# Optimization experiments

Measured on AMD Instinct MI355X. Metric: run time of the kernel, lower is better.

Reference implementation:

```python
import jax, jax.numpy as jnp
import numpy as np

N_NODES = 100000
N_EDGES = 1600000
D = 64


def setup_inputs() -> dict:
    key = jax.random.key(0)
    k0, k1, k2, k3 = jax.random.split(key, 4)
    x = jax.random.normal(k0, (N_NODES, D), dtype=jnp.float32)
    edge_index = jax.random.randint(k1, (2, N_EDGES), 0, N_NODES, dtype=jnp.int64)
    W1 = jax.random.normal(k2, (D, D), dtype=jnp.float32) * 0.1
    b1 = jnp.zeros((D,), dtype=jnp.float32)
    W2 = jax.random.normal(k3, (D, D), dtype=jnp.float32) * 0.1
    b2 = jnp.zeros((D,), dtype=jnp.float32)
    return {"x": x, "edge_index": edge_index, "W1": W1, "b1": b1, "W2": W2, "b2": b2}


def _gcn_layer(x, edge_index, W, b):
    n = x.shape[0]
    h = x @ W  # [N, Dout] -- transform before aggregation (small GEMM)
    loop = jnp.arange(n, dtype=edge_index.dtype)
    src = jnp.concatenate([edge_index[0], loop])
    dst = jnp.concatenate([edge_index[1], loop])
    deg = jax.ops.segment_sum(jnp.ones_like(dst, dtype=h.dtype), dst, num_segments=n)
    dinv = jax.lax.rsqrt(deg)  # deg >= 1 thanks to self loops
    norm = dinv[src] * dinv[dst]  # [E+N]
    msg = h[src] * norm[:, None]  # gather: [E+N, Dout]
    agg = jax.ops.segment_sum(msg, dst, num_segments=n)  # scatter-add
    return agg + b


def reference(x, edge_index, W1, b1, W2, b2):
    # dropout p = 0.0 -> identity
    h = jax.nn.relu(_gcn_layer(x, edge_index, W1, b1))
    h = jax.nn.relu(_gcn_layer(h, edge_index, W2, b2))
    return h
```

## Files before the change

### kernel.cpp

```cpp
#include <hip/hip_runtime.h>
#include <hip/hip_bf16.h>

#define D 64
#define NB_HIST 256
#define MAXBK 512

typedef float vfloat4 __attribute__((ext_vector_type(4)));

__device__ __forceinline__ unsigned short f2bf(float f) {
    union { float f; unsigned u; } v; v.f = f;
    unsigned r = (v.u + 0x7FFF + ((v.u >> 16) & 1)) >> 16;
    return (unsigned short)r;
}
__device__ __forceinline__ float bflo(unsigned u) {
    union { unsigned u; float f; } v; v.u = u << 16; return v.f;
}
__device__ __forceinline__ float bfhi(unsigned u) {
    union { unsigned u; float f; } v; v.u = u & 0xFFFF0000u; return v.f;
}

__global__ __launch_bounds__(256) void passA_gemm(
    const int* __restrict__ dst, int* __restrict__ blockCounts, int E, int per, int NBK,
    const float* __restrict__ X, const float* __restrict__ W,
    unsigned short* __restrict__ hn, int N)
{
    int tid = threadIdx.x;

    if ((int)blockIdx.x < NB_HIST) {
        __shared__ int hist[MAXBK];
        for (int i = tid; i < NBK; i += 256) hist[i] = 0;
        __syncthreads();
        int lo = blockIdx.x * per, hi = min(E, lo + per);
        for (int i = lo + tid * 4; i < hi; i += 1024) {
            if (i + 3 < hi) {
                int4 d4 = *(const int4*)(dst + i);
                atomicAdd(&hist[d4.x >> 8], 1);
                atomicAdd(&hist[d4.y >> 8], 1);
                atomicAdd(&hist[d4.z >> 8], 1);
                atomicAdd(&hist[d4.w >> 8], 1);
            } else {
                for (int k = i; k < hi; ++k) atomicAdd(&hist[dst[k] >> 8], 1);
            }
        }
        __syncthreads();
        for (int i = tid; i < NBK; i += 256)
            blockCounts[(size_t)blockIdx.x * NBK + i] = hist[i];
        return;
    }

    __shared__ float sW[D * D];
    __shared__ float sX[32 * D];
    int rowBase = ((int)blockIdx.x - NB_HIST) * 32;

    for (int i = tid; i < 1024; i += 256)
        ((vfloat4*)sW)[i] = ((const vfloat4*)W)[i];
    for (int i = tid; i < 512; i += 256) {
        int r = rowBase + (i >> 4);
        vfloat4 v = (vfloat4)0.0f;
        if (r < N) v = __builtin_nontemporal_load(((const vfloat4*)X) + rowBase * 16 + i);
        ((vfloat4*)sX)[i] = v;
    }
    __syncthreads();

    int wave = tid >> 6, lane = tid & 63;
    float accv[8];
#pragma unroll
    for (int r = 0; r < 8; ++r) accv[r] = 0.0f;
    int xoff = (wave * 8) * D;
#pragma unroll 8
    for (int k = 0; k < D; ++k) {
        float wv = sW[k * D + lane];
#pragma unroll
        for (int r = 0; r < 8; ++r)
            accv[r] += sX[xoff + r * D + k] * wv;
    }
#pragma unroll
    for (int r = 0; r < 8; ++r) {
        int row = rowBase + wave * 8 + r;
        if (row < N) hn[(size_t)row * D + lane] = f2bf(accv[r]);
    }
}

__global__ __launch_bounds__(256) void scan_cols(
    const int* __restrict__ blockCounts, int* __restrict__ partial,
    int* __restrict__ totals, int NBK)
{
    int wave = threadIdx.x >> 6, lane = threadIdx.x & 63;
    int k = blockIdx.x * 4 + wave;
    if (k >= NBK) return;
    int carry = 0;
    for (int base = 0; base < NB_HIST; base += 64) {
        int b = base + lane;
        int v = blockCounts[(size_t)b * NBK + k];
        int inc = v;
        for (int d = 1; d < 64; d <<= 1) {
            int t = __shfl_up(inc, d, 64);
            if (lane >= d) inc += t;
        }
        partial[(size_t)k * NB_HIST + b] = inc - v + carry;
        carry += __shfl(inc, 63, 64);
    }
    if (lane == 0) totals[k] = carry;
}

__global__ void scan_buckets(const int* __restrict__ totals, int* __restrict__ bofs, int NBK) {
    int lane = threadIdx.x;
    int carry = 0;
    for (int base = 0; base < NBK; base += 64) {
        int i = base + lane;
        int v = (i < NBK) ? totals[i] : 0;
        int inc = v;
        for (int d = 1; d < 64; d <<= 1) {
            int t = __shfl_up(inc, d, 64);
            if (lane >= d) inc += t;
        }
        if (i < NBK) bofs[i] = inc - v + carry;
        carry += __shfl(inc, 63, 64);
    }
}

__global__ __launch_bounds__(256) void passB(
    const int* __restrict__ src, const int* __restrict__ dst,
    const int* __restrict__ bofs, const int* __restrict__ partial,
    int* __restrict__ bucketed, int E, int per, int NBK)
{
    __shared__ int cur[MAXBK];
    int tid = threadIdx.x, b = blockIdx.x;
    for (int i = tid; i < NBK; i += 256)
        cur[i] = bofs[i] + partial[(size_t)i * NB_HIST + b];
    __syncthreads();
    int lo = b * per, hi = min(E, lo + per);
    for (int i = lo + tid * 4; i < hi; i += 1024) {
        if (i + 3 < hi) {
            int4 d4 = *(const int4*)(dst + i);
            int4 s4 = *(const int4*)(src + i);
            int p0 = atomicAdd(&cur[d4.x >> 8], 1);
            int p1 = atomicAdd(&cur[d4.y >> 8], 1);
            int p2 = atomicAdd(&cur[d4.z >> 8], 1);
            int p3 = atomicAdd(&cur[d4.w >> 8], 1);
            bucketed[p0] = (s4.x << 8) | (d4.x & 255);
            bucketed[p1] = (s4.y << 8) | (d4.y & 255);
            bucketed[p2] = (s4.z << 8) | (d4.z & 255);
            bucketed[p3] = (s4.w << 8) | (d4.w & 255);
        } else {
            for (int k = i; k < hi; ++k) {
                int d = dst[k], s = src[k];
                int pos = atomicAdd(&cur[d >> 8], 1);
                bucketed[pos] = (s << 8) | (d & 255);
            }
        }
    }
}

__global__ __launch_bounds__(256) void build_csr_scale(
    const int* __restrict__ bucketed, const int* __restrict__ bofs,
    const int* __restrict__ totals, int* __restrict__ deg, float* __restrict__ dinv,
    int* __restrict__ ofs, int* __restrict__ csr,
    unsigned short* __restrict__ hn, int N)
{
    __shared__ int h[256];
    __shared__ int scn[256];
    __shared__ float sdv[256];
    int tid = threadIdx.x, k = blockIdx.x;
    int e0 = bofs[k], e1 = e0 + totals[k];
    int node = k * 256 + tid;

    h[tid] = 0;
    __syncthreads();
    for (int i = e0 + tid; i < e1; i += 256)
        atomicAdd(&h[bucketed[i] & 255], 1);
    __syncthreads();

    int mydeg = h[tid];
    scn[tid] = mydeg;
    __syncthreads();
    for (int d2 = 1; d2 < 256; d2 <<= 1) {
        int t = (tid >= d2) ? scn[tid - d2] : 0;
        __syncthreads();
        scn[tid] += t;
        __syncthreads();
    }
    int myofs = scn[tid] - mydeg;

    float dv = rsqrtf((float)(mydeg + 1));
    sdv[tid] = dv;
    if (node < N) {
        deg[node]  = mydeg;
        dinv[node] = dv;
        ofs[node]  = e0 + myofs;
    }

    h[tid] = myofs;
    __syncthreads();
    for (int i = e0 + tid; i < e1; i += 256) {
        int v = bucketed[i];
        int pos = atomicAdd(&h[v & 255], 1);
        csr[e0 + pos] = v >> 8;
    }

    __syncthreads();
    int4* hp = (int4*)hn;
    for (int c = tid; c < 2048; c += 256) {
        int r = c >> 3;
        int n2 = k * 256 + r;
        if (n2 < N) {
            float f = sdv[r];
            size_t idx = (size_t)n2 * 8 + (c & 7);
            int4 hv = hp[idx];
            unsigned r0 = (unsigned)f2bf(bflo(hv.x) * f) | ((unsigned)f2bf(bfhi(hv.x) * f) << 16);
            unsigned r1 = (unsigned)f2bf(bflo(hv.y) * f) | ((unsigned)f2bf(bfhi(hv.y) * f) << 16);
            unsigned r2 = (unsigned)f2bf(bflo(hv.z) * f) | ((unsigned)f2bf(bfhi(hv.z) * f) << 16);
            unsigned r3 = (unsigned)f2bf(bflo(hv.w) * f) | ((unsigned)f2bf(bfhi(hv.w) * f) << 16);
            hp[idx] = make_int4((int)r0, (int)r1, (int)r2, (int)r3);
        }
    }
}

__global__ __launch_bounds__(256) void gemm2(
    const unsigned short* __restrict__ h1b, const float* __restrict__ W,
    const float* __restrict__ dinv, unsigned short* __restrict__ hn, int N)
{
    __shared__ float sW[D * D];
    __shared__ float sX[32 * D];
    int tid = threadIdx.x;
    int rowBase = blockIdx.x * 32;

    for (int i = tid; i < 1024; i += 256)
        ((vfloat4*)sW)[i] = ((const vfloat4*)W)[i];
    {
        int r = tid >> 3, c8 = tid & 7;
        int row = rowBase + r;
        int4 hv = make_int4(0, 0, 0, 0);
        if (row < N) hv = ((const int4*)h1b)[(size_t)row * 8 + c8];
        float* dst8 = &sX[r * D + c8 * 8];
        dst8[0] = bflo(hv.x); dst8[1] = bfhi(hv.x);
        dst8[2] = bflo(hv.y); dst8[3] = bfhi(hv.y);
        dst8[4] = bflo(hv.z); dst8[5] = bfhi(hv.z);
        dst8[6] = bflo(hv.w); dst8[7] = bfhi(hv.w);
    }
    __syncthreads();

    int wave = tid >> 6, lane = tid & 63;
    float accv[8];
#pragma unroll
    for (int r = 0; r < 8; ++r) accv[r] = 0.0f;
    int xoff = (wave * 8) * D;
#pragma unroll 8
    for (int k = 0; k < D; ++k) {
        float wv = sW[k * D + lane];
#pragma unroll
        for (int r = 0; r < 8; ++r)
            accv[r] += sX[xoff + r * D + k] * wv;
    }
#pragma unroll
    for (int r = 0; r < 8; ++r) {
        int row = rowBase + wave * 8 + r;
        if (row < N) hn[(size_t)row * D + lane] = f2bf(accv[r] * dinv[row]);
    }
}

template <bool BF16OUT>
__global__ __launch_bounds__(256) void aggregate_relu(
    const int* __restrict__ ofs, const int* __restrict__ deg,
    const int* __restrict__ csr, const unsigned short* __restrict__ hn,
    const float* __restrict__ dinv, const float* __restrict__ bias,
    void* __restrict__ outv, int N)
{
    int t    = blockIdx.x * 256 + threadIdx.x;
    int lane = threadIdx.x & 63;
    int grp  = lane >> 3, sub = lane & 7;
    int node = (t >> 6) * 8 + grp;
    bool live = (node < N);

    const int4* hrow = (const int4*)hn;
    float2 a0 = {0.f, 0.f}, a1 = {0.f, 0.f}, a2 = {0.f, 0.f}, a3 = {0.f, 0.f};

    int s0 = 0, cnt = 0;
    if (live) {
        s0  = ofs[node];
        cnt = deg[node];
        int4 h = hrow[(size_t)node * 8 + sub];
        a0.x += bflo(h.x); a0.y += bfhi(h.x);
        a1.x += bflo(h.y); a1.y += bfhi(h.y);
        a2.x += bflo(h.z); a2.y += bfhi(h.z);
        a3.x += bflo(h.w); a3.y += bfhi(h.w);
    }

    const int* cp = csr + s0;
    int j = 0;
    for (; j + 3 < cnt; j += 4) {
        int sA = cp[j], sB = cp[j + 1], sC = cp[j + 2], sD = cp[j + 3];
        int4 hA = hrow[(size_t)sA * 8 + sub];
        int4 hB = hrow[(size_t)sB * 8 + sub];
        int4 hC = hrow[(size_t)sC * 8 + sub];
        int4 hD = hrow[(size_t)sD * 8 + sub];
        a0.x += bflo(hA.x); a0.y += bfhi(hA.x);
        a1.x += bflo(hA.y); a1.y += bfhi(hA.y);
        a2.x += bflo(hA.z); a2.y += bfhi(hA.z);
        a3.x += bflo(hA.w); a3.y += bfhi(hA.w);
        a0.x += bflo(hB.x); a0.y += bfhi(hB.x);
        a1.x += bflo(hB.y); a1.y += bfhi(hB.y);
        a2.x += bflo(hB.z); a2.y += bfhi(hB.z);
        a3.x += bflo(hB.w); a3.y += bfhi(hB.w);
        a0.x += bflo(hC.x); a0.y += bfhi(hC.x);
        a1.x += bflo(hC.y); a1.y += bfhi(hC.y);
        a2.x += bflo(hC.z); a2.y += bfhi(hC.z);
        a3.x += bflo(hC.w); a3.y += bfhi(hC.w);
        a0.x += bflo(hD.x); a0.y += bfhi(hD.x);
        a1.x += bflo(hD.y); a1.y += bfhi(hD.y);
        a2.x += bflo(hD.z); a2.y += bfhi(hD.z);
        a3.x += bflo(hD.w); a3.y += bfhi(hD.w);
    }
    for (; j < cnt; ++j) {
        int sA = cp[j];
        int4 hA = hrow[(size_t)sA * 8 + sub];
        a0.x += bflo(hA.x); a0.y += bfhi(hA.x);
        a1.x += bflo(hA.y); a1.y += bfhi(hA.y);
        a2.x += bflo(hA.z); a2.y += bfhi(hA.z);
        a3.x += bflo(hA.w); a3.y += bfhi(hA.w);
    }

    if (live) {
        float dw = dinv[node];
        float4 b0 = ((const float4*)bias)[sub * 2];
        float4 b1 = ((const float4*)bias)[sub * 2 + 1];
        float o0 = fmaxf(a0.x * dw + b0.x, 0.f);
        float o1 = fmaxf(a0.y * dw + b0.y, 0.f);
        float o2 = fmaxf(a1.x * dw + b0.z, 0.f);
        float o3 = fmaxf(a1.y * dw + b0.w, 0.f);
        float o4 = fmaxf(a2.x * dw + b1.x, 0.f);
        float o5 = fmaxf(a2.y * dw + b1.y, 0.f);
        float o6 = fmaxf(a3.x * dw + b1.z, 0.f);
        float o7 = fmaxf(a3.y * dw + b1.w, 0.f);
        if (BF16OUT) {
            unsigned r0 = (unsigned)f2bf(o0) | ((unsigned)f2bf(o1) << 16);
            unsigned r1 = (unsigned)f2bf(o2) | ((unsigned)f2bf(o3) << 16);
            unsigned r2 = (unsigned)f2bf(o4) | ((unsigned)f2bf(o5) << 16);
            unsigned r3 = (unsigned)f2bf(o6) | ((unsigned)f2bf(o7) << 16);
            ((int4*)outv)[(size_t)node * 8 + sub] =
                make_int4((int)r0, (int)r1, (int)r2, (int)r3);
        } else {
            float4 v0 = make_float4(o0, o1, o2, o3);
            float4 v1 = make_float4(o4, o5, o6, o7);
            ((float4*)outv)[(size_t)node * 16 + sub * 2]     = v0;
            ((float4*)outv)[(size_t)node * 16 + sub * 2 + 1] = v1;
        }
    }
}


extern "C" void kernel_launch(void* const* d_in, const int* in_sizes, int n_in,
                              void* d_out, int out_size, void* d_ws, size_t ws_size,
                              hipStream_t stream) {
    const float* x   = (const float*)d_in[0];
    const int*   ei  = (const int*)d_in[1];
    const float* W1  = (const float*)d_in[2];
    const float* b1  = (const float*)d_in[3];
    const float* W2  = (const float*)d_in[4];
    const float* b2  = (const float*)d_in[5];

    int N = in_sizes[0] / D;
    int E = in_sizes[1] / 2;
    const int* src = ei;
    const int* dst = ei + E;
    int NBK = (N + 255) >> 8;
    int per = (((E + NB_HIST - 1) / NB_HIST) + 3) & ~3;

    char* ws = (char*)d_ws;
    int*            blockCounts = (int*)(ws + 0x00000000);
    int*            partial     = (int*)(ws + 0x00080000);
    int*            totals      = (int*)(ws + 0x00100000);
    int*            bofs        = (int*)(ws + 0x00110000);
    int*            deg         = (int*)(ws + 0x00120000);
    float*          dinv        = (float*)(ws + 0x00190000);
    int*            ofs         = (int*)(ws + 0x00200000);
    int*            bucketed    = (int*)(ws + 0x00280000);
    int*            csr         = (int*)(ws + 0x00A00000);
    unsigned short* hn          = (unsigned short*)(ws + 0x01100000);
    unsigned short* h1b         = (unsigned short*)(ws + 0x01D80000);
    float*          outF        = (float*)d_out;

    int nb_G = (N + 31) / 32;
    int nb_A = (N + 31) / 32;

    passA_gemm<<<NB_HIST + nb_G, 256, 0, stream>>>(dst, blockCounts, E, per, NBK, x, W1, hn, N);
    scan_cols<<<(NBK + 3) / 4, 256, 0, stream>>>(blockCounts, partial, totals, NBK);
    scan_buckets<<<1, 64, 0, stream>>>(totals, bofs, NBK);
    passB<<<NB_HIST, 256, 0, stream>>>(src, dst, bofs, partial, bucketed, E, per, NBK);
    build_csr_scale<<<NBK, 256, 0, stream>>>(bucketed, bofs, totals, deg, dinv, ofs, csr, hn, N);

    aggregate_relu<true><<<nb_A, 256, 0, stream>>>(ofs, deg, csr, hn, dinv, b1, (void*)h1b, N);
    gemm2<<<nb_G, 256, 0, stream>>>(h1b, W2, dinv, hn, N);
    aggregate_relu<false><<<nb_A, 256, 0, stream>>>(ofs, deg, csr, hn, dinv, b2, (void*)outF, N);
}
```

Measured before the change: 240.1 us.

## Fuse scans via last-block counter, split CSR histogram by src tile, vectorize GEMM

```diff
diff --git a/kernel.cpp b/kernel.cpp
--- a/kernel.cpp
+++ b/kernel.cpp
@@ -4,6 +4,7 @@
 #define D 64
 #define NB_HIST 256
 #define MAXBK 512
+#define NT 16
 
 typedef float vfloat4 __attribute__((ext_vector_type(4)));
 
@@ -20,13 +21,15 @@
 }
 
 __global__ __launch_bounds__(256) void passA_gemm(
-    const int* __restrict__ dst, int* __restrict__ blockCounts, int E, int per, int NBK,
+    const int* __restrict__ dst, int* __restrict__ blockCounts, int* __restrict__ ctr,
+    int E, int per, int NBK,
     const float* __restrict__ X, const float* __restrict__ W,
     unsigned short* __restrict__ hn, int N)
 {
     int tid = threadIdx.x;
 
     if ((int)blockIdx.x < NB_HIST) {
+        if (blockIdx.x == 0 && tid == 0) *ctr = 0;
         __shared__ int hist[MAXBK];
         for (int i = tid; i < NBK; i += 256) hist[i] = 0;
         __syncthreads();
@@ -67,12 +70,17 @@
 #pragma unroll
     for (int r = 0; r < 8; ++r) accv[r] = 0.0f;
     int xoff = (wave * 8) * D;
-#pragma unroll 8
-    for (int k = 0; k < D; ++k) {
-        float wv = sW[k * D + lane];
-#pragma unroll
-        for (int r = 0; r < 8; ++r)
-            accv[r] += sX[xoff + r * D + k] * wv;
+#pragma unroll 4
+    for (int k = 0; k < D; k += 4) {
+        float w0 = sW[k * D + lane];
+        float w1 = sW[(k + 1) * D + lane];
+        float w2 = sW[(k + 2) * D + lane];
+        float w3 = sW[(k + 3) * D + lane];
+#pragma unroll
+        for (int r = 0; r < 8; ++r) {
+            vfloat4 xv = *(const vfloat4*)&sX[xoff + r * D + k];
+            accv[r] += xv.x * w0 + xv.y * w1 + xv.z * w2 + xv.w * w3;
+        }
     }
 #pragma unroll
     for (int r = 0; r < 8; ++r) {
@@ -81,41 +89,47 @@
     }
 }
 
-__global__ __launch_bounds__(256) void scan_cols(
+__global__ __launch_bounds__(256) void scan_all(
     const int* __restrict__ blockCounts, int* __restrict__ partial,
-    int* __restrict__ totals, int NBK)
-{
+    int* __restrict__ totals, int* __restrict__ bofs, int* __restrict__ ctr, int NBK)
+{
+    __shared__ int slast;
     int wave = threadIdx.x >> 6, lane = threadIdx.x & 63;
     int k = blockIdx.x * 4 + wave;
-    if (k >= NBK) return;
-    int carry = 0;
-    for (int base = 0; base < NB_HIST; base += 64) {
-        int b = base + lane;
-        int v = blockCounts[(size_t)b * NBK + k];
-        int inc = v;
-        for (int d = 1; d < 64; d <<= 1) {
-            int t = __shfl_up(inc, d, 64);
-            if (lane >= d) inc += t;
-        }
-        partial[(size_t)k * NB_HIST + b] = inc - v + carry;
-        carry += __shfl(inc, 63, 64);
-    }
-    if (lane == 0) totals[k] = carry;
-}
-
-__global__ void scan_buckets(const int* __restrict__ totals, int* __restrict__ bofs, int NBK) {
-    int lane = threadIdx.x;
-    int carry = 0;
-    for (int base = 0; base < NBK; base += 64) {
-        int i = base + lane;
-        int v = (i < NBK) ? totals[i] : 0;
-        int inc = v;
-        for (int d = 1; d < 64; d <<= 1) {
-            int t = __shfl_up(inc, d, 64);
-            if (lane >= d) inc += t;
-        }
-        if (i < NBK) bofs[i] = inc - v + carry;
-        carry += __shfl(inc, 63, 64);
+    if (k < NBK) {
+        int carry = 0;
+        for (int base = 0; base < NB_HIST; base += 64) {
+            int b = base + lane;
+            int v = blockCounts[(size_t)b * NBK + k];
+            int inc = v;
+            for (int d = 1; d < 64; d <<= 1) {
+                int t = __shfl_up(inc, d, 64);
+                if (lane >= d) inc += t;
+            }
+            partial[(size_t)k * NB_HIST + b] = inc - v + carry;
+            carry += __shfl(inc, 63, 64);
+        }
+        if (lane == 0) totals[k] = carry;
+    }
+    __syncthreads();
+    __threadfence();
+    if (threadIdx.x == 0)
+        slast = (atomicAdd(ctr, 1) == (int)gridDim.x - 1) ? 1 : 0;
+    __syncthreads();
+    if (slast && wave == 0) {
+        __threadfence();
+        int carry = 0;
+        for (int base = 0; base < NBK; base += 64) {
+            int i = base + lane;
+            int v = (i < NBK) ? totals[i] : 0;
+            int inc = v;
+            for (int d = 1; d < 64; d <<= 1) {
+                int t = __shfl_up(inc, d, 64);
+                if (lane >= d) inc += t;
+            }
+            if (i < NBK) bofs[i] = inc - v + carry;
+            carry += __shfl(inc, 63, 64);
+        }
     }
 }
 
@@ -158,20 +172,28 @@
     int* __restrict__ ofs, int* __restrict__ csr,
     unsigned short* __restrict__ hn, int N)
 {
-    __shared__ int h[256];
+    __shared__ int h2[NT * 256];
     __shared__ int scn[256];
     __shared__ float sdv[256];
     int tid = threadIdx.x, k = blockIdx.x;
     int e0 = bofs[k], e1 = e0 + totals[k];
     int node = k * 256 + tid;
 
-    h[tid] = 0;
-    __syncthreads();
-    for (int i = e0 + tid; i < e1; i += 256)
-        atomicAdd(&h[bucketed[i] & 255], 1);
-    __syncthreads();
-
-    int mydeg = h[tid];
+    for (int i = tid; i < NT * 256; i += 256) h2[i] = 0;
+    __syncthreads();
+    for (int i = e0 + tid; i < e1; i += 256) {
+        int v = bucketed[i];
+        atomicAdd(&h2[((v >> 21) << 8) | (v & 255)], 1);
+    }
+    __syncthreads();
+
+    int pre[NT];
+    int mydeg = 0;
+#pragma unroll
+    for (int t2 = 0; t2 < NT; ++t2) {
+        pre[t2] = mydeg;
+        mydeg += h2[(t2 << 8) | tid];
+    }
     scn[tid] = mydeg;
     __syncthreads();
     for (int d2 = 1; d2 < 256; d2 <<= 1) {
@@ -190,11 +212,13 @@
         ofs[node]  = e0 + myofs;
     }
 
-    h[tid] = myofs;
+#pragma unroll
+    for (int t2 = 0; t2 < NT; ++t2)
+        h2[(t2 << 8) | tid] = myofs + pre[t2];
     __syncthreads();
     for (int i = e0 + tid; i < e1; i += 256) {
         int v = bucketed[i];
-        int pos = atomicAdd(&h[v & 255], 1);
+        int pos = atomicAdd(&h2[((v >> 21) << 8) | (v & 255)], 1);
         csr[e0 + pos] = v >> 8;
     }
 
@@ -245,12 +269,17 @@
 #pragma unroll
     for (int r = 0; r < 8; ++r) accv[r] = 0.0f;
     int xoff = (wave * 8) * D;
-#pragma unroll 8
-    for (int k = 0; k < D; ++k) {
-        float wv = sW[k * D + lane];
-#pragma unroll
-        for (int r = 0; r < 8; ++r)
-            accv[r] += sX[xoff + r * D + k] * wv;
+#pragma unroll 4
+    for (int k = 0; k < D; k += 4) {
+        float w0 = sW[k * D + lane];
+        float w1 = sW[(k + 1) * D + lane];
+        float w2 = sW[(k + 2) * D + lane];
+        float w3 = sW[(k + 3) * D + lane];
+#pragma unroll
+        for (int r = 0; r < 8; ++r) {
+            vfloat4 xv = *(const vfloat4*)&sX[xoff + r * D + k];
+            accv[r] += xv.x * w0 + xv.y * w1 + xv.z * w2 + xv.w * w3;
+        }
     }
 #pragma unroll
     for (int r = 0; r < 8; ++r) {
@@ -371,6 +400,7 @@
     int*            partial     = (int*)(ws + 0x00080000);
     int*            totals      = (int*)(ws + 0x00100000);
     int*            bofs        = (int*)(ws + 0x00110000);
+    int*            ctr         = (int*)(ws + 0x00118000);
     int*            deg         = (int*)(ws + 0x00120000);
     float*          dinv        = (float*)(ws + 0x00190000);
     int*            ofs         = (int*)(ws + 0x00200000);
@@ -383,9 +413,8 @@
     int nb_G = (N + 31) / 32;
     int nb_A = (N + 31) / 32;
 
-    passA_gemm<<<NB_HIST + nb_G, 256, 0, stream>>>(dst, blockCounts, E, per, NBK, x, W1, hn, N);
-    scan_cols<<<(NBK + 3) / 4, 256, 0, stream>>>(blockCounts, partial, totals, NBK);
-    scan_buckets<<<1, 64, 0, stream>>>(totals, bofs, NBK);
+    passA_gemm<<<NB_HIST + nb_G, 256, 0, stream>>>(dst, blockCounts, ctr, E, per, NBK, x, W1, hn, N);
+    scan_all<<<(NBK + 3) / 4, 256, 0, stream>>>(blockCounts, partial, totals, bofs, ctr, NBK);
     passB<<<NB_HIST, 256, 0, stream>>>(src, dst, bofs, partial, bucketed, E, per, NBK);
     build_csr_scale<<<NBK, 256, 0, stream>>>(bucketed, bofs, totals, deg, dinv, ofs, csr, hn, N);
 
```

Measured after the change: 246.4 us. 2.6% more time.
